# Kernel tuning notes

Hardware: AMD Instinct MI355X
Metric: run time of the kernel (lower is better)

The kernel has to match this reference:

```python
import jax, jax.numpy as jnp
import numpy as np

B, S, IN_F, OUT_F = 4, 2048, 4096, 4096
ALPHA = 0.01

def setup_inputs() -> dict:
    key = jax.random.key(0)
    k1, k2 = jax.random.split(key, 2)
    # int8-valued activations and weights (stored as int32 per harness dtype)
    x = jax.random.randint(k1, (B, S, IN_F), -127, 127, dtype=jnp.int32)
    weight = jax.random.randint(k2, (IN_F, OUT_F), -127, 127, dtype=jnp.int32)
    bias = jnp.zeros((1, OUT_F), dtype=jnp.float16)
    alpha = jnp.full((1,), ALPHA, dtype=jnp.float32)
    return {"x": x, "weight": weight, "bias": bias, "alpha": alpha}

def reference(x, weight, bias, alpha):
    # Faithful to forward's default (non-hybrid) path:
    # y = F.linear(x.float(), weight.t().float(), bias.float()) * alpha
    # F.linear(x, W^T) == x @ W, with W shape (in_features, out_features).
    x_shape = x.shape
    xf = x.reshape(-1, x_shape[-1]).astype(jnp.float32)          # [B*S, in]
    wf = weight.astype(jnp.float32)                               # [in, out]
    y = (xf @ wf + bias.astype(jnp.float32)) * alpha              # [B*S, out]
    return y.reshape(*x_shape[:-1], -1)                           # [B, S, out]
```

## Files before the change

kernel.cpp:

```cpp
#include <hip/hip_runtime.h>
#include <hip/hip_fp16.h>

using i32x4  = __attribute__((ext_vector_type(4)))  int;
using i32x16 = __attribute__((ext_vector_type(16))) int;

static constexpr int M  = 4 * 2048;
static constexpr int N  = 4096;
static constexpr int K  = 4096;
static constexpr int BM = 256, BN = 256, BK = 64;
static constexpr int NT = K / BK;
static constexpr int TILE = BM * BK;


__device__ __forceinline__ unsigned pack4(i32x4 v) {
  return (unsigned)((v.x & 255) | ((v.y & 255) << 8) | ((v.z & 255) << 16) | (v.w << 24));
}

__global__ __launch_bounds__(256) void pack_x_kernel(const int* __restrict__ x,
                                                     unsigned char* __restrict__ wa) {
  unsigned g = blockIdx.x * 256 + threadIdx.x;
  unsigned row = g & 255;
  unsigned kg  = (g >> 8) & 3;
  unsigned kt  = (g >> 10) & 63;
  unsigned br  = g >> 16;
  const int* src = x + ((size_t)(br * 256 + row) * K + kt * 64 + kg * 16);
  i32x4 v0 = *(const i32x4*)(src + 0);
  i32x4 v1 = *(const i32x4*)(src + 4);
  i32x4 v2 = *(const i32x4*)(src + 8);
  i32x4 v3 = *(const i32x4*)(src + 12);
  i32x4 d;
  d.x = (int)pack4(v0); d.y = (int)pack4(v1); d.z = (int)pack4(v2); d.w = (int)pack4(v3);
  *(i32x4*)(wa + (size_t)g * 16) = d;
}

__global__ __launch_bounds__(256) void pack_w_kernel(const int* __restrict__ w,
                                                     unsigned char* __restrict__ wb) {
  unsigned g = blockIdx.x * 256 + threadIdx.x;
  unsigned col = g & 255;
  unsigned kg  = (g >> 8) & 3;
  unsigned kt  = (g >> 10) & 63;
  unsigned bn  = g >> 16;
  unsigned n   = bn * 256 + col;
  unsigned k0  = kt * 64 + kg * 16;
  const int* src = w + (size_t)k0 * N + n;
  i32x4 d;
#pragma unroll
  for (int j = 0; j < 4; ++j) {
    int b0 = src[(size_t)(j * 4 + 0) * N];
    int b1 = src[(size_t)(j * 4 + 1) * N];
    int b2 = src[(size_t)(j * 4 + 2) * N];
    int b3 = src[(size_t)(j * 4 + 3) * N];
    d[j] = (b0 & 255) | ((b1 & 255) << 8) | ((b2 & 255) << 16) | (b3 << 24);
  }
  *(i32x4*)(wb + (size_t)g * 16) = d;
}


__device__ __forceinline__ void gload_lds16(const void* g, void* l) {
  __builtin_amdgcn_global_load_lds((const __attribute__((address_space(1))) unsigned int*)g,
                                   (__attribute__((address_space(3))) unsigned int*)l,
                                   16, 0, 0);
}

#define FENCE()   asm volatile("" ::: "memory")
#define BARRIER() do { FENCE(); __builtin_amdgcn_s_barrier(); FENCE(); } while (0)

__global__ __launch_bounds__(512, 2) void gemm_i8(const unsigned char* __restrict__ wa,
                                                  const unsigned char* __restrict__ wb,
                                                  const __half* __restrict__ bias,
                                                  const float* __restrict__ alphaP,
                                                  float* __restrict__ out) {
  __shared__ __align__(16) unsigned char As[3][TILE];
  __shared__ __align__(16) unsigned char Bs[3][TILE];

  const int tid  = threadIdx.x;
  const int lane = tid & 63;
  const int w    = tid >> 6;
  const int wr   = w >> 2, wc = w & 3;
  const int l31  = lane & 31;
  const int kgl  = lane >> 5;

  const int bid = blockIdx.x;
  const int swz = (bid & 7) * 64 + (bid >> 3);
  const int bc  = swz & 15;
  const int br  = swz >> 4;

  const unsigned char* ga = wa + (size_t)br * NT * TILE;
  const unsigned char* gb = wb + (size_t)bc * NT * TILE;

  auto stage = [&](int buf, int t) {
    const unsigned char* at = ga + (size_t)t * TILE;
    const unsigned char* bt = gb + (size_t)t * TILE;
    gload_lds16(at + w * 1024 + lane * 16,        &As[buf][w * 1024]);
    gload_lds16(at + 8192 + w * 1024 + lane * 16, &As[buf][8192 + w * 1024]);
    gload_lds16(bt + w * 1024 + lane * 16,        &Bs[buf][w * 1024]);
    gload_lds16(bt + 8192 + w * 1024 + lane * 16, &Bs[buf][8192 + w * 1024]);
  };

  stage(0, 0);
  stage(1, 1);
  stage(2, 2);

  i32x16 acc[4][2] = {};

  int buf = 0;
  for (int t = 0; t < NT; ++t) {
    if (t + 2 < NT)      asm volatile("s_waitcnt vmcnt(8)" ::: "memory");
    else if (t + 1 < NT) asm volatile("s_waitcnt vmcnt(4)" ::: "memory");
    else                 asm volatile("s_waitcnt vmcnt(0)" ::: "memory");
    BARRIER();

    i32x4 a[2][4], b[2][2];
#pragma unroll
    for (int kc = 0; kc < 2; ++kc) {
      const int kg = kc * 2 + kgl;
      const unsigned char* Ap = &As[buf][kg * 4096];
      const unsigned char* Bp = &Bs[buf][kg * 4096];
#pragma unroll
      for (int mi = 0; mi < 4; ++mi)
        a[kc][mi] = *(const i32x4*)(Ap + (wr * 128 + mi * 32 + l31) * 16);
#pragma unroll
      for (int ni = 0; ni < 2; ++ni)
        b[kc][ni] = *(const i32x4*)(Bp + (wc * 64 + ni * 32 + l31) * 16);
    }
    asm volatile("s_waitcnt lgkmcnt(0)" ::: "memory");
    BARRIER();
    if (t + 3 < NT) stage(buf, t + 3);

    __builtin_amdgcn_s_setprio(1);
#pragma unroll
    for (int kc = 0; kc < 2; ++kc)
#pragma unroll
      for (int mi = 0; mi < 4; ++mi)
#pragma unroll
        for (int ni = 0; ni < 2; ++ni)
          acc[mi][ni] = __builtin_amdgcn_mfma_i32_32x32x32_i8(a[kc][mi], b[kc][ni],
                                                              acc[mi][ni], 0, 0, 0);
    __builtin_amdgcn_s_setprio(0);

    buf = (buf == 2) ? 0 : buf + 1;
  }

  const float alpha = *alphaP;
  const int row0 = br * 256 + wr * 128 + 4 * kgl;
  const int col0 = bc * 256 + wc * 64 + l31;
#pragma unroll
  for (int ni = 0; ni < 2; ++ni) {
    const int col = col0 + ni * 32;
    const float bf = __half2float(bias[col]);
#pragma unroll
    for (int mi = 0; mi < 4; ++mi) {
#pragma unroll
      for (int r = 0; r < 16; ++r) {
        const int row = row0 + mi * 32 + (r & 3) + 8 * (r >> 2);
        out[(size_t)row * N + col] = ((float)acc[mi][ni][r] + bf) * alpha;
      }
    }
  }
}

extern "C" void kernel_launch(void* const* d_in, const int* in_sizes, int n_in,
                              void* d_out, int out_size, void* d_ws, size_t ws_size,
                              hipStream_t stream) {
  const int*    x     = (const int*)d_in[0];
  const int*    wgt   = (const int*)d_in[1];
  const __half* bias  = (const __half*)d_in[2];
  const float*  alpha = (const float*)d_in[3];
  float*        out   = (float*)d_out;

  unsigned char* wa = (unsigned char*)d_ws;
  unsigned char* wb = wa + (size_t)M * K;

  pack_x_kernel<<<(M * (size_t)K / 16) / 256, 256, 0, stream>>>(x, wa);
  pack_w_kernel<<<(N * (size_t)K / 16) / 256, 256, 0, stream>>>(wgt, wb);

  dim3 grid((M / BM) * (N / BN));
  gemm_i8<<<grid, 512, 0, stream>>>(wa, wb, bias, alpha, out);
}
```

Measured before the change: 231.3 us.

## Interleave LDS reads, MFMA and global prefetch in four phases per K tile

Restructures the main loop into four phases per K tile. Each phase issues a few LDS fragment reads and one quarter of the next-next tile's global-to-LDS copy, then runs four MFMAs between barriers. Prefetch depth drops from three tiles ahead to two, while keeping the three LDS buffers. This spreads memory traffic across the MFMA work and cuts register pressure from the fragment arrays, at the cost of many more barriers per iteration.

```diff
diff --git a/kernel.cpp b/kernel.cpp
--- a/kernel.cpp
+++ b/kernel.cpp
@@ -62,9 +62,6 @@
                                    16, 0, 0);
 }
 
-#define FENCE()   asm volatile("" ::: "memory")
-#define BARRIER() do { FENCE(); __builtin_amdgcn_s_barrier(); FENCE(); } while (0)
-
 __global__ __launch_bounds__(512, 2) void gemm_i8(const unsigned char* __restrict__ wa,
                                                   const unsigned char* __restrict__ wb,
                                                   const __half* __restrict__ bias,
@@ -88,57 +85,94 @@
   const unsigned char* ga = wa + (size_t)br * NT * TILE;
   const unsigned char* gb = wb + (size_t)bc * NT * TILE;
 
-  auto stage = [&](int buf, int t) {
-    const unsigned char* at = ga + (size_t)t * TILE;
-    const unsigned char* bt = gb + (size_t)t * TILE;
-    gload_lds16(at + w * 1024 + lane * 16,        &As[buf][w * 1024]);
-    gload_lds16(at + 8192 + w * 1024 + lane * 16, &As[buf][8192 + w * 1024]);
-    gload_lds16(bt + w * 1024 + lane * 16,        &Bs[buf][w * 1024]);
-    gload_lds16(bt + 8192 + w * 1024 + lane * 16, &Bs[buf][8192 + w * 1024]);
+  auto stage_q = [&](int buf, int t, int q) {
+    const unsigned char* src = (q < 2 ? ga : gb) + (size_t)t * TILE + (q & 1) * 8192;
+    unsigned char*       dst = (q < 2 ? As[buf] : Bs[buf]) + (q & 1) * 8192;
+    gload_lds16(src + w * 1024 + lane * 16, dst + w * 1024);
   };
 
-  stage(0, 0);
-  stage(1, 1);
-  stage(2, 2);
+#pragma unroll
+  for (int q = 0; q < 4; ++q) stage_q(0, 0, q);
+#pragma unroll
+  for (int q = 0; q < 4; ++q) stage_q(1, 1, q);
 
   i32x16 acc[4][2] = {};
 
-  int buf = 0;
+  asm volatile("s_waitcnt vmcnt(4)" ::: "memory");
+  __builtin_amdgcn_s_barrier();
+
+  const int arow = wr * 128 + l31;
+  const int bcol = wc * 64 + l31;
+
   for (int t = 0; t < NT; ++t) {
-    if (t + 2 < NT)      asm volatile("s_waitcnt vmcnt(8)" ::: "memory");
-    else if (t + 1 < NT) asm volatile("s_waitcnt vmcnt(4)" ::: "memory");
-    else                 asm volatile("s_waitcnt vmcnt(0)" ::: "memory");
-    BARRIER();
-
-    i32x4 a[2][4], b[2][2];
-#pragma unroll
-    for (int kc = 0; kc < 2; ++kc) {
-      const int kg = kc * 2 + kgl;
-      const unsigned char* Ap = &As[buf][kg * 4096];
-      const unsigned char* Bp = &Bs[buf][kg * 4096];
-#pragma unroll
-      for (int mi = 0; mi < 4; ++mi)
-        a[kc][mi] = *(const i32x4*)(Ap + (wr * 128 + mi * 32 + l31) * 16);
-#pragma unroll
-      for (int ni = 0; ni < 2; ++ni)
-        b[kc][ni] = *(const i32x4*)(Bp + (wc * 64 + ni * 32 + l31) * 16);
-    }
-    asm volatile("s_waitcnt lgkmcnt(0)" ::: "memory");
-    BARRIER();
-    if (t + 3 < NT) stage(buf, t + 3);
-
-    __builtin_amdgcn_s_setprio(1);
-#pragma unroll
-    for (int kc = 0; kc < 2; ++kc)
-#pragma unroll
-      for (int mi = 0; mi < 4; ++mi)
-#pragma unroll
-        for (int ni = 0; ni < 2; ++ni)
-          acc[mi][ni] = __builtin_amdgcn_mfma_i32_32x32x32_i8(a[kc][mi], b[kc][ni],
-                                                              acc[mi][ni], 0, 0, 0);
-    __builtin_amdgcn_s_setprio(0);
-
-    buf = (buf == 2) ? 0 : buf + 1;
+    const unsigned char* Abase = As[t % 3] + kgl * 4096;
+    const unsigned char* Bbase = Bs[t % 3] + kgl * 4096;
+    const bool pf   = (t + 2 < NT);
+    const int  pbuf = (t + 2) % 3;
+
+    i32x4 a0, a1, a2, a3, b0, b1;
+
+    a0 = *(const i32x4*)(Abase + (arow +  0) * 16);
+    a1 = *(const i32x4*)(Abase + (arow + 32) * 16);
+    b0 = *(const i32x4*)(Bbase + (bcol +  0) * 16);
+    b1 = *(const i32x4*)(Bbase + (bcol + 32) * 16);
+    if (pf) stage_q(pbuf, t + 2, 0);
+    __builtin_amdgcn_s_barrier();
+    asm volatile("s_waitcnt lgkmcnt(0)" ::: "memory");
+    __builtin_amdgcn_sched_barrier(0);
+    __builtin_amdgcn_s_setprio(1);
+    acc[0][0] = __builtin_amdgcn_mfma_i32_32x32x32_i8(a0, b0, acc[0][0], 0, 0, 0);
+    acc[0][1] = __builtin_amdgcn_mfma_i32_32x32x32_i8(a0, b1, acc[0][1], 0, 0, 0);
+    acc[1][0] = __builtin_amdgcn_mfma_i32_32x32x32_i8(a1, b0, acc[1][0], 0, 0, 0);
+    acc[1][1] = __builtin_amdgcn_mfma_i32_32x32x32_i8(a1, b1, acc[1][1], 0, 0, 0);
+    __builtin_amdgcn_s_setprio(0);
+    __builtin_amdgcn_s_barrier();
+
+    a2 = *(const i32x4*)(Abase + (arow + 64) * 16);
+    a3 = *(const i32x4*)(Abase + (arow + 96) * 16);
+    if (pf) stage_q(pbuf, t + 2, 1);
+    __builtin_amdgcn_s_barrier();
+    asm volatile("s_waitcnt lgkmcnt(0)" ::: "memory");
+    __builtin_amdgcn_sched_barrier(0);
+    __builtin_amdgcn_s_setprio(1);
+    acc[2][0] = __builtin_amdgcn_mfma_i32_32x32x32_i8(a2, b0, acc[2][0], 0, 0, 0);
+    acc[2][1] = __builtin_amdgcn_mfma_i32_32x32x32_i8(a2, b1, acc[2][1], 0, 0, 0);
+    acc[3][0] = __builtin_amdgcn_mfma_i32_32x32x32_i8(a3, b0, acc[3][0], 0, 0, 0);
+    acc[3][1] = __builtin_amdgcn_mfma_i32_32x32x32_i8(a3, b1, acc[3][1], 0, 0, 0);
+    __builtin_amdgcn_s_setprio(0);
+    __builtin_amdgcn_s_barrier();
+
+    a0 = *(const i32x4*)(Abase + 8192 + (arow +  0) * 16);
+    a1 = *(const i32x4*)(Abase + 8192 + (arow + 32) * 16);
+    b0 = *(const i32x4*)(Bbase + 8192 + (bcol +  0) * 16);
+    b1 = *(const i32x4*)(Bbase + 8192 + (bcol + 32) * 16);
+    if (pf) stage_q(pbuf, t + 2, 2);
+    __builtin_amdgcn_s_barrier();
+    asm volatile("s_waitcnt lgkmcnt(0)" ::: "memory");
+    __builtin_amdgcn_sched_barrier(0);
+    __builtin_amdgcn_s_setprio(1);
+    acc[0][0] = __builtin_amdgcn_mfma_i32_32x32x32_i8(a0, b0, acc[0][0], 0, 0, 0);
+    acc[0][1] = __builtin_amdgcn_mfma_i32_32x32x32_i8(a0, b1, acc[0][1], 0, 0, 0);
+    acc[1][0] = __builtin_amdgcn_mfma_i32_32x32x32_i8(a1, b0, acc[1][0], 0, 0, 0);
+    acc[1][1] = __builtin_amdgcn_mfma_i32_32x32x32_i8(a1, b1, acc[1][1], 0, 0, 0);
+    __builtin_amdgcn_s_setprio(0);
+    __builtin_amdgcn_s_barrier();
+
+    a2 = *(const i32x4*)(Abase + 8192 + (arow + 64) * 16);
+    a3 = *(const i32x4*)(Abase + 8192 + (arow + 96) * 16);
+    if (pf) stage_q(pbuf, t + 2, 3);
+    __builtin_amdgcn_s_barrier();
+    asm volatile("s_waitcnt lgkmcnt(0)" ::: "memory");
+    __builtin_amdgcn_sched_barrier(0);
+    __builtin_amdgcn_s_setprio(1);
+    acc[2][0] = __builtin_amdgcn_mfma_i32_32x32x32_i8(a2, b0, acc[2][0], 0, 0, 0);
+    acc[2][1] = __builtin_amdgcn_mfma_i32_32x32x32_i8(a2, b1, acc[2][1], 0, 0, 0);
+    acc[3][0] = __builtin_amdgcn_mfma_i32_32x32x32_i8(a3, b0, acc[3][0], 0, 0, 0);
+    acc[3][1] = __builtin_amdgcn_mfma_i32_32x32x32_i8(a3, b1, acc[3][1], 0, 0, 0);
+    __builtin_amdgcn_s_setprio(0);
+    if (t + 2 < NT)      asm volatile("s_waitcnt vmcnt(4)" ::: "memory");
+    else if (t + 1 < NT) asm volatile("s_waitcnt vmcnt(0)" ::: "memory");
+    __builtin_amdgcn_s_barrier();
   }
 
   const float alpha = *alphaP;
```

New measurement: 266.5 us. 15.2% more time.

## Load B fragments directly to registers and restructure A pipeline with one barrier

Applied to the files above, without the earlier changes.

B tiles are no longer staged through LDS; each wave loads its B fragments straight from global memory into double-buffered registers one tile ahead. A keeps a 3-deep LDS ring, now prefetched two tiles ahead, with one barrier per step instead of two, and its LDS reads are split so the second k-half is read while the first half's MFMAs run. The block-to-tile swizzle is also changed. This cuts LDS traffic and barrier stalls, at the cost of redundant global/L2 reads of B across the two wave rows and more VGPR pressure.

```diff
diff --git a/kernel.cpp b/kernel.cpp
--- a/kernel.cpp
+++ b/kernel.cpp
@@ -62,16 +62,12 @@
                                    16, 0, 0);
 }
 
-#define FENCE()   asm volatile("" ::: "memory")
-#define BARRIER() do { FENCE(); __builtin_amdgcn_s_barrier(); FENCE(); } while (0)
-
 __global__ __launch_bounds__(512, 2) void gemm_i8(const unsigned char* __restrict__ wa,
                                                   const unsigned char* __restrict__ wb,
                                                   const __half* __restrict__ bias,
                                                   const float* __restrict__ alphaP,
                                                   float* __restrict__ out) {
   __shared__ __align__(16) unsigned char As[3][TILE];
-  __shared__ __align__(16) unsigned char Bs[3][TILE];
 
   const int tid  = threadIdx.x;
   const int lane = tid & 63;
@@ -81,64 +77,73 @@
   const int kgl  = lane >> 5;
 
   const int bid = blockIdx.x;
-  const int swz = (bid & 7) * 64 + (bid >> 3);
-  const int bc  = swz & 15;
-  const int br  = swz >> 4;
+  const int i   = bid >> 3;
+  const int bc  = (bid & 7) * 2 + (i >> 5);
+  const int br  = i & 31;
 
   const unsigned char* ga = wa + (size_t)br * NT * TILE;
   const unsigned char* gb = wb + (size_t)bc * NT * TILE;
 
-  auto stage = [&](int buf, int t) {
+  const int arow = wr * 128 + l31;
+  const int bcol = wc * 64 + l31;
+
+  auto stageA = [&](int buf, int t) {
     const unsigned char* at = ga + (size_t)t * TILE;
-    const unsigned char* bt = gb + (size_t)t * TILE;
     gload_lds16(at + w * 1024 + lane * 16,        &As[buf][w * 1024]);
     gload_lds16(at + 8192 + w * 1024 + lane * 16, &As[buf][8192 + w * 1024]);
-    gload_lds16(bt + w * 1024 + lane * 16,        &Bs[buf][w * 1024]);
-    gload_lds16(bt + 8192 + w * 1024 + lane * 16, &Bs[buf][8192 + w * 1024]);
   };
 
-  stage(0, 0);
-  stage(1, 1);
-  stage(2, 2);
+  i32x4 breg[2][2][2];
+
+#define LOADB(PAR, T) do {                                                   \
+    const unsigned char* bt = gb + (size_t)(T) * TILE;                       \
+    breg[PAR][0][0] = *(const i32x4*)(bt + (0 + kgl) * 4096 + (bcol +  0) * 16); \
+    breg[PAR][0][1] = *(const i32x4*)(bt + (0 + kgl) * 4096 + (bcol + 32) * 16); \
+    breg[PAR][1][0] = *(const i32x4*)(bt + (2 + kgl) * 4096 + (bcol +  0) * 16); \
+    breg[PAR][1][1] = *(const i32x4*)(bt + (2 + kgl) * 4096 + (bcol + 32) * 16); \
+  } while (0)
+
+  stageA(0, 0);
+  LOADB(0, 0);
+  stageA(1, 1);
+  asm volatile("s_waitcnt vmcnt(2)" ::: "memory");
+  __builtin_amdgcn_s_barrier();
 
   i32x16 acc[4][2] = {};
 
-  int buf = 0;
-  for (int t = 0; t < NT; ++t) {
-    if (t + 2 < NT)      asm volatile("s_waitcnt vmcnt(8)" ::: "memory");
-    else if (t + 1 < NT) asm volatile("s_waitcnt vmcnt(4)" ::: "memory");
-    else                 asm volatile("s_waitcnt vmcnt(0)" ::: "memory");
-    BARRIER();
+#define MFMA(mi, ni, AF, PAR, KC)                                            \
+  acc[mi][ni] = __builtin_amdgcn_mfma_i32_32x32x32_i8(AF, breg[PAR][KC][ni], \
+                                                      acc[mi][ni], 0, 0, 0)
 
-    i32x4 a[2][4], b[2][2];
-#pragma unroll
-    for (int kc = 0; kc < 2; ++kc) {
-      const int kg = kc * 2 + kgl;
-      const unsigned char* Ap = &As[buf][kg * 4096];
-      const unsigned char* Bp = &Bs[buf][kg * 4096];
-#pragma unroll
-      for (int mi = 0; mi < 4; ++mi)
-        a[kc][mi] = *(const i32x4*)(Ap + (wr * 128 + mi * 32 + l31) * 16);
-#pragma unroll
-      for (int ni = 0; ni < 2; ++ni)
-        b[kc][ni] = *(const i32x4*)(Bp + (wc * 64 + ni * 32 + l31) * 16);
-    }
-    asm volatile("s_waitcnt lgkmcnt(0)" ::: "memory");
-    BARRIER();
-    if (t + 3 < NT) stage(buf, t + 3);
+#define STEP(T, PAR) do {                                                    \
+    const unsigned char* Ab = &As[(T) % 3][0] + kgl * 4096;                  \
+    i32x4 a0 = *(const i32x4*)(Ab + (arow +  0) * 16);                       \
+    i32x4 a1 = *(const i32x4*)(Ab + (arow + 32) * 16);                       \
+    i32x4 a2 = *(const i32x4*)(Ab + (arow + 64) * 16);                       \
+    i32x4 a3 = *(const i32x4*)(Ab + (arow + 96) * 16);                       \
+    if ((T) + 1 < NT) LOADB(PAR ^ 1, (T) + 1);           \
+    if ((T) + 2 < NT) stageA(((T) + 2) % 3, (T) + 2);     \
+    MFMA(0, 0, a0, PAR, 0); MFMA(0, 1, a0, PAR, 0);                          \
+    MFMA(1, 0, a1, PAR, 0); MFMA(1, 1, a1, PAR, 0);                          \
+    MFMA(2, 0, a2, PAR, 0); MFMA(2, 1, a2, PAR, 0);                          \
+    MFMA(3, 0, a3, PAR, 0); MFMA(3, 1, a3, PAR, 0);                          \
+    i32x4 c0 = *(const i32x4*)(Ab + 8192 + (arow +  0) * 16);                \
+    i32x4 c1 = *(const i32x4*)(Ab + 8192 + (arow + 32) * 16);                \
+    i32x4 c2 = *(const i32x4*)(Ab + 8192 + (arow + 64) * 16);                \
+    i32x4 c3 = *(const i32x4*)(Ab + 8192 + (arow + 96) * 16);                \
+    MFMA(0, 0, c0, PAR, 1); MFMA(0, 1, c0, PAR, 1);                          \
+    MFMA(1, 0, c1, PAR, 1); MFMA(1, 1, c1, PAR, 1);                          \
+    MFMA(2, 0, c2, PAR, 1); MFMA(2, 1, c2, PAR, 1);                          \
+    MFMA(3, 0, c3, PAR, 1); MFMA(3, 1, c3, PAR, 1);                          \
+    \
+    if ((T) + 2 < NT)      asm volatile("s_waitcnt vmcnt(2)" ::: "memory");  \
+    else if ((T) + 1 < NT) asm volatile("s_waitcnt vmcnt(0)" ::: "memory");  \
+    if ((T) + 1 < NT) __builtin_amdgcn_s_barrier();                          \
+  } while (0)
 
-    __builtin_amdgcn_s_setprio(1);
-#pragma unroll
-    for (int kc = 0; kc < 2; ++kc)
-#pragma unroll
-      for (int mi = 0; mi < 4; ++mi)
-#pragma unroll
-        for (int ni = 0; ni < 2; ++ni)
-          acc[mi][ni] = __builtin_amdgcn_mfma_i32_32x32x32_i8(a[kc][mi], b[kc][ni],
-                                                              acc[mi][ni], 0, 0, 0);
-    __builtin_amdgcn_s_setprio(0);
-
-    buf = (buf == 2) ? 0 : buf + 1;
+  for (int t = 0; t < NT; t += 2) {
+    STEP(t, 0);
+    STEP(t + 1, 1);
   }
 
   const float alpha = *alphaP;
@@ -157,6 +162,9 @@
       }
     }
   }
+#undef STEP
+#undef MFMA
+#undef LOADB
 }
 
 extern "C" void kernel_launch(void* const* d_in, const int* in_sizes, int n_in,
```

New measurement: 248.6 us. 7.5% more time.

## Use 4-wave blocks with 128x128 warp tiles and single-barrier prefetch pipeline

Applied to the files above, without the earlier changes.

Halves the block to 256 threads so each wave computes a 128x128 tile with 16 accumulators, which raises register-level reuse of the A and B fragments. The triple-buffered pipeline now prefetches two tiles ahead and uses one barrier per iteration instead of two. It also interleaves the LDS reads of the two k-halves with their MFMA groups, and changes the block-to-tile swizzle. In exchange, each wave needs many more accumulator registers, occupancy drops to a single block of 4 waves per CU, and there are fewer waves available to hide latency.

```diff
diff --git a/kernel.cpp b/kernel.cpp
--- a/kernel.cpp
+++ b/kernel.cpp
@@ -62,10 +62,7 @@
                                    16, 0, 0);
 }
 
-#define FENCE()   asm volatile("" ::: "memory")
-#define BARRIER() do { FENCE(); __builtin_amdgcn_s_barrier(); FENCE(); } while (0)
-
-__global__ __launch_bounds__(512, 2) void gemm_i8(const unsigned char* __restrict__ wa,
+__global__ __launch_bounds__(256, 1) void gemm_i8(const unsigned char* __restrict__ wa,
                                                   const unsigned char* __restrict__ wb,
                                                   const __half* __restrict__ bias,
                                                   const float* __restrict__ alphaP,
@@ -76,14 +73,14 @@
   const int tid  = threadIdx.x;
   const int lane = tid & 63;
   const int w    = tid >> 6;
-  const int wr   = w >> 2, wc = w & 3;
+  const int wr   = w >> 1, wc = w & 1;
   const int l31  = lane & 31;
   const int kgl  = lane >> 5;
 
   const int bid = blockIdx.x;
-  const int swz = (bid & 7) * 64 + (bid >> 3);
-  const int bc  = swz & 15;
-  const int br  = swz >> 4;
+  const int i   = bid >> 3;
+  const int bc  = (bid & 7) * 2 + (i >> 5);
+  const int br  = i & 31;
 
   const unsigned char* ga = wa + (size_t)br * NT * TILE;
   const unsigned char* gb = wb + (size_t)bc * NT * TILE;
@@ -91,61 +88,80 @@
   auto stage = [&](int buf, int t) {
     const unsigned char* at = ga + (size_t)t * TILE;
     const unsigned char* bt = gb + (size_t)t * TILE;
-    gload_lds16(at + w * 1024 + lane * 16,        &As[buf][w * 1024]);
-    gload_lds16(at + 8192 + w * 1024 + lane * 16, &As[buf][8192 + w * 1024]);
-    gload_lds16(bt + w * 1024 + lane * 16,        &Bs[buf][w * 1024]);
-    gload_lds16(bt + 8192 + w * 1024 + lane * 16, &Bs[buf][8192 + w * 1024]);
+#pragma unroll
+    for (int j = 0; j < 4; ++j) {
+      gload_lds16(at + w * 4096 + j * 1024 + lane * 16, &As[buf][w * 4096 + j * 1024]);
+      gload_lds16(bt + w * 4096 + j * 1024 + lane * 16, &Bs[buf][w * 4096 + j * 1024]);
+    }
   };
 
   stage(0, 0);
   stage(1, 1);
-  stage(2, 2);
+  asm volatile("s_waitcnt vmcnt(8)" ::: "memory");
+  __builtin_amdgcn_s_barrier();
 
-  i32x16 acc[4][2] = {};
+  i32x16 acc[4][4] = {};
 
-  int buf = 0;
+  const int arow = wr * 128 + l31;
+  const int bcol = wc * 128 + l31;
+
   for (int t = 0; t < NT; ++t) {
+    const unsigned char* Ab = &As[t % 3][0] + kgl * 4096;
+    const unsigned char* Bb = &Bs[t % 3][0] + kgl * 4096;
+
+    if (t + 2 < NT) stage((t + 2) % 3, t + 2);
+
+    i32x4 a0 = *(const i32x4*)(Ab + (arow +  0) * 16);
+    i32x4 a1 = *(const i32x4*)(Ab + (arow + 32) * 16);
+    i32x4 a2 = *(const i32x4*)(Ab + (arow + 64) * 16);
+    i32x4 a3 = *(const i32x4*)(Ab + (arow + 96) * 16);
+    i32x4 b0 = *(const i32x4*)(Bb + (bcol +  0) * 16);
+    i32x4 b1 = *(const i32x4*)(Bb + (bcol + 32) * 16);
+    i32x4 b2 = *(const i32x4*)(Bb + (bcol + 64) * 16);
+    i32x4 b3 = *(const i32x4*)(Bb + (bcol + 96) * 16);
+
+#define MFMA16(A0, A1, A2, A3, B0, B1, B2, B3)                                 \
+    acc[0][0] = __builtin_amdgcn_mfma_i32_32x32x32_i8(A0, B0, acc[0][0], 0,0,0); \
+    acc[0][1] = __builtin_amdgcn_mfma_i32_32x32x32_i8(A0, B1, acc[0][1], 0,0,0); \
+    acc[0][2] = __builtin_amdgcn_mfma_i32_32x32x32_i8(A0, B2, acc[0][2], 0,0,0); \
+    acc[0][3] = __builtin_amdgcn_mfma_i32_32x32x32_i8(A0, B3, acc[0][3], 0,0,0); \
+    acc[1][0] = __builtin_amdgcn_mfma_i32_32x32x32_i8(A1, B0, acc[1][0], 0,0,0); \
+    acc[1][1] = __builtin_amdgcn_mfma_i32_32x32x32_i8(A1, B1, acc[1][1], 0,0,0); \
+    acc[1][2] = __builtin_amdgcn_mfma_i32_32x32x32_i8(A1, B2, acc[1][2], 0,0,0); \
+    acc[1][3] = __builtin_amdgcn_mfma_i32_32x32x32_i8(A1, B3, acc[1][3], 0,0,0); \
+    acc[2][0] = __builtin_amdgcn_mfma_i32_32x32x32_i8(A2, B0, acc[2][0], 0,0,0); \
+    acc[2][1] = __builtin_amdgcn_mfma_i32_32x32x32_i8(A2, B1, acc[2][1], 0,0,0); \
+    acc[2][2] = __builtin_amdgcn_mfma_i32_32x32x32_i8(A2, B2, acc[2][2], 0,0,0); \
+    acc[2][3] = __builtin_amdgcn_mfma_i32_32x32x32_i8(A2, B3, acc[2][3], 0,0,0); \
+    acc[3][0] = __builtin_amdgcn_mfma_i32_32x32x32_i8(A3, B0, acc[3][0], 0,0,0); \
+    acc[3][1] = __builtin_amdgcn_mfma_i32_32x32x32_i8(A3, B1, acc[3][1], 0,0,0); \
+    acc[3][2] = __builtin_amdgcn_mfma_i32_32x32x32_i8(A3, B2, acc[3][2], 0,0,0); \
+    acc[3][3] = __builtin_amdgcn_mfma_i32_32x32x32_i8(A3, B3, acc[3][3], 0,0,0)
+
+    MFMA16(a0, a1, a2, a3, b0, b1, b2, b3);
+
+    a0 = *(const i32x4*)(Ab + 8192 + (arow +  0) * 16);
+    a1 = *(const i32x4*)(Ab + 8192 + (arow + 32) * 16);
+    a2 = *(const i32x4*)(Ab + 8192 + (arow + 64) * 16);
+    a3 = *(const i32x4*)(Ab + 8192 + (arow + 96) * 16);
+    b0 = *(const i32x4*)(Bb + 8192 + (bcol +  0) * 16);
+    b1 = *(const i32x4*)(Bb + 8192 + (bcol + 32) * 16);
+    b2 = *(const i32x4*)(Bb + 8192 + (bcol + 64) * 16);
+    b3 = *(const i32x4*)(Bb + 8192 + (bcol + 96) * 16);
+
+    MFMA16(a0, a1, a2, a3, b0, b1, b2, b3);
+#undef MFMA16
+
     if (t + 2 < NT)      asm volatile("s_waitcnt vmcnt(8)" ::: "memory");
-    else if (t + 1 < NT) asm volatile("s_waitcnt vmcnt(4)" ::: "memory");
-    else                 asm volatile("s_waitcnt vmcnt(0)" ::: "memory");
-    BARRIER();
-
-    i32x4 a[2][4], b[2][2];
-#pragma unroll
-    for (int kc = 0; kc < 2; ++kc) {
-      const int kg = kc * 2 + kgl;
-      const unsigned char* Ap = &As[buf][kg * 4096];
-      const unsigned char* Bp = &Bs[buf][kg * 4096];
-#pragma unroll
-      for (int mi = 0; mi < 4; ++mi)
-        a[kc][mi] = *(const i32x4*)(Ap + (wr * 128 + mi * 32 + l31) * 16);
-#pragma unroll
-      for (int ni = 0; ni < 2; ++ni)
-        b[kc][ni] = *(const i32x4*)(Bp + (wc * 64 + ni * 32 + l31) * 16);
-    }
-    asm volatile("s_waitcnt lgkmcnt(0)" ::: "memory");
-    BARRIER();
-    if (t + 3 < NT) stage(buf, t + 3);
-
-    __builtin_amdgcn_s_setprio(1);
-#pragma unroll
-    for (int kc = 0; kc < 2; ++kc)
-#pragma unroll
-      for (int mi = 0; mi < 4; ++mi)
-#pragma unroll
-        for (int ni = 0; ni < 2; ++ni)
-          acc[mi][ni] = __builtin_amdgcn_mfma_i32_32x32x32_i8(a[kc][mi], b[kc][ni],
-                                                              acc[mi][ni], 0, 0, 0);
-    __builtin_amdgcn_s_setprio(0);
-
-    buf = (buf == 2) ? 0 : buf + 1;
+    else if (t + 1 < NT) asm volatile("s_waitcnt vmcnt(0)" ::: "memory");
+    __builtin_amdgcn_s_barrier();
   }
 
   const float alpha = *alphaP;
   const int row0 = br * 256 + wr * 128 + 4 * kgl;
-  const int col0 = bc * 256 + wc * 64 + l31;
+  const int col0 = bc * 256 + wc * 128 + l31;
 #pragma unroll
-  for (int ni = 0; ni < 2; ++ni) {
+  for (int ni = 0; ni < 4; ++ni) {
     const int col = col0 + ni * 32;
     const float bf = __half2float(bias[col]);
 #pragma unroll
@@ -175,5 +191,5 @@
   pack_w_kernel<<<(N * (size_t)K / 16) / 256, 256, 0, stream>>>(wgt, wb);
 
   dim3 grid((M / BM) * (N / BN));
-  gemm_i8<<<grid, 512, 0, stream>>>(wa, wb, bias, alpha, out);
+  gemm_i8<<<grid, 256, 0, stream>>>(wa, wb, bias, alpha, out);
 }
```

New measurement: 261.0 us. 1.13x slower.
